# Kernel optimization log

Hardware: AMD Instinct MI355X
Metric: run time of the kernel (lower is better)

Reference implementation:

```python
import jax, jax.numpy as jnp
import numpy as np


def setup_inputs() -> dict:
    key = jax.random.key(0)
    k1, k2 = jax.random.split(key)
    B, d, h = 65536, 256, 1024  # na = d//4 = 64, G = B//na = 1024, h = 4*d
    x = jax.random.normal(k1, (B, d), dtype=jnp.float32)
    A = 0.1 * jax.random.normal(k2, (d, h), dtype=jnp.float32)
    return {"x": x, "A": A}


def reference(x, A):
    # x: [B, d], A: [d, h] with h = 4*d, na = d // 4, G = B // na
    B, d = x.shape
    na = d // 4
    G = B // na
    n2 = 2 * na

    # bmm with broadcast A + SiLU -> [B, h]; reshape [B, 16, na], sum -> [B]
    J = jax.nn.silu(x @ A)                      # [B, h]
    j12 = J.reshape(B, 16, na).sum(axis=(1, 2)).reshape(G, na)  # [G, na]

    # kron(diag(j12), eye(2)) duplicates each diagonal entry onto a 2x2 identity
    diagvals = jnp.repeat(j12, 2, axis=1)        # [G, 2*na]

    # Final block matrix [[J11, J12], [J21, J22]] with J11=J22=0,
    # J12 = +diag, J21 = -diag, each expanded by kron with eye(2).
    idx = jnp.arange(n2)
    out = jnp.zeros((G, 4 * na, 4 * na), dtype=x.dtype)
    out = out.at[:, idx, n2 + idx].set(diagvals)    # top-right block diagonal
    out = out.at[:, n2 + idx, idx].set(-diagvals)   # bottom-left block diagonal
    return out
```

## Files before the change

kernel.cpp:

```cpp
#include <hip/hip_runtime.h>
#include <stdint.h>

typedef float    f32x4  __attribute__((ext_vector_type(4)));
typedef __bf16   bf16x8 __attribute__((ext_vector_type(8)));
typedef uint32_t u32x4  __attribute__((ext_vector_type(4)));
typedef unsigned short u16x4 __attribute__((ext_vector_type(4)));

#define AS1 __attribute__((address_space(1)))
#define AS3 __attribute__((address_space(3)))

__device__ __forceinline__ unsigned short f2bf_bits(float f) {
  uint32_t u = __builtin_bit_cast(uint32_t, f);
  u += 0x7fffu + ((u >> 16) & 1u);
  return (unsigned short)(u >> 16);
}

__global__ void k_transpose_cvt(const float* __restrict__ A,
                                unsigned short* __restrict__ At) {
  int n = blockIdx.x * blockDim.x + threadIdx.x;
  int o = n << 2;
  int col = o >> 8;
  int k   = o & 255;
  u16x4 v;
#pragma unroll
  for (int j = 0; j < 4; ++j) v[j] = f2bf_bits(A[(size_t)(k + j) * 1024 + col]);
  *reinterpret_cast<u16x4*>(At + o) = v;
}

__launch_bounds__(256, 2)
__global__ void k_gemm_fused(const float* __restrict__ x,
                             const unsigned short* __restrict__ At,
                             float* __restrict__ out) {
  __shared__ alignas(16) char lds[8192];

  const int tid  = threadIdx.x;
  const int lane = tid & 63;
  const int w    = tid >> 6;
  const int bIdx = blockIdx.x;
  const int brow = bIdx * 128;

  const int col = lane & 15;
  const int hi  = lane >> 4;

  bf16x8 xf[2][8];
#pragma unroll
  for (int rg = 0; rg < 2; ++rg) {
    const float* xr = x + (size_t)(brow + w * 32 + rg * 16 + col) * 256;
#pragma unroll
    for (int s = 0; s < 8; ++s) {
      f32x4 a = __builtin_nontemporal_load(
          reinterpret_cast<const f32x4*>(xr + s * 32 + hi * 8));
      f32x4 b = __builtin_nontemporal_load(
          reinterpret_cast<const f32x4*>(xr + s * 32 + hi * 8 + 4));
      bf16x8 f;
      f[0] = (__bf16)a[0]; f[1] = (__bf16)a[1];
      f[2] = (__bf16)a[2]; f[3] = (__bf16)a[3];
      f[4] = (__bf16)b[0]; f[5] = (__bf16)b[1];
      f[6] = (__bf16)b[2]; f[7] = (__bf16)b[3];
      xf[rg][s] = f;
    }
  }

  uint32_t p0 = (uint32_t)(w * 2048 + lane * 16);
  uint32_t so0 = p0 ^ (((p0 >> 9) & 7u) << 4);
  uint32_t p1 = p0 + 1024u;
  uint32_t so1 = p1 ^ (((p1 >> 9) & 7u) << 4);
  char* ldsw0 = lds + w * 2048;
  char* ldsw1 = lds + w * 2048 + 1024;

  uint32_t rbase = ((uint32_t)(col * 512 + hi * 16)) ^ ((uint32_t)(col & 7) << 4);

  float sums[2][4] = {{0.f, 0.f, 0.f, 0.f}, {0.f, 0.f, 0.f, 0.f}};
  float* outblk = out + (size_t)bIdx * 131072;
  const f32x4 z4 = {0.f, 0.f, 0.f, 0.f};

  for (int tile = 0; tile < 64; ++tile) {
    const char* tsrc = (const char*)At + (size_t)tile * 8192;
    __builtin_amdgcn_global_load_lds((const AS1 uint32_t*)(tsrc + so0),
                                     (AS3 uint32_t*)ldsw0, 16, 0, 0);
    __builtin_amdgcn_global_load_lds((const AS1 uint32_t*)(tsrc + so1),
                                     (AS3 uint32_t*)ldsw1, 16, 0, 0);

    float* zp = outblk + tile * 2048 + (tid << 2);
    __builtin_nontemporal_store(z4, reinterpret_cast<f32x4*>(zp));
    __builtin_nontemporal_store(z4, reinterpret_cast<f32x4*>(zp + 1024));

    __syncthreads();

    bf16x8 bfr[8];
#pragma unroll
    for (int s = 0; s < 8; ++s) {
      uint32_t addr = rbase ^ ((uint32_t)s << 6);
      bfr[s] = __builtin_bit_cast(
          bf16x8, *reinterpret_cast<const u32x4*>(lds + addr));
    }
    f32x4 acc[2] = {{0.f, 0.f, 0.f, 0.f}, {0.f, 0.f, 0.f, 0.f}};
#pragma unroll
    for (int s = 0; s < 8; ++s) {
      acc[0] = __builtin_amdgcn_mfma_f32_16x16x32_bf16(xf[0][s], bfr[s], acc[0], 0, 0, 0);
      acc[1] = __builtin_amdgcn_mfma_f32_16x16x32_bf16(xf[1][s], bfr[s], acc[1], 0, 0, 0);
    }
#pragma unroll
    for (int rg = 0; rg < 2; ++rg)
#pragma unroll
      for (int j = 0; j < 4; ++j) {
        float z = acc[rg][j];
        float sig = __builtin_amdgcn_rcpf(1.0f + __expf(-z));
        sums[rg][j] += z * sig;
      }
    __syncthreads();
  }

#pragma unroll
  for (int rg = 0; rg < 2; ++rg)
#pragma unroll
    for (int j = 0; j < 4; ++j) {
      float v = sums[rg][j];
      v += __shfl_xor(v, 1, 64);
      v += __shfl_xor(v, 2, 64);
      v += __shfl_xor(v, 4, 64);
      v += __shfl_xor(v, 8, 64);
      sums[rg][j] = v;
    }

  if (col == 0) {
#pragma unroll
    for (int rg = 0; rg < 2; ++rg)
#pragma unroll
      for (int j = 0; j < 4; ++j) {
        int rb_ = brow + w * 32 + rg * 16 + hi * 4 + j;
        int g = rb_ >> 6;
        int c = rb_ & 63;
        float s = sums[rg][j];
        float* og = out + (size_t)g * 65536;
        og[(2 * c) * 256 + 128 + 2 * c]     =  s;
        og[(2 * c + 1) * 256 + 129 + 2 * c] =  s;
        og[(128 + 2 * c) * 256 + 2 * c]     = -s;
        og[(129 + 2 * c) * 256 + 2 * c + 1] = -s;
      }
  }
}

extern "C" void kernel_launch(void* const* d_in, const int* in_sizes, int n_in,
                              void* d_out, int out_size, void* d_ws, size_t ws_size,
                              hipStream_t stream) {
  const float* x = (const float*)d_in[0];
  const float* A = (const float*)d_in[1];
  float* out = (float*)d_out;
  unsigned short* At = (unsigned short*)d_ws;

  k_transpose_cvt<<<256, 256, 0, stream>>>(A, At);
  k_gemm_fused<<<512, 256, 0, stream>>>(x, At, out);
}
```

Before: 79.24 us.

## Multi-buffer A tiles in LDS with two-tile-ahead prefetch

```diff
diff --git a/kernel.cpp b/kernel.cpp
--- a/kernel.cpp
+++ b/kernel.cpp
@@ -31,7 +31,7 @@
 __global__ void k_gemm_fused(const float* __restrict__ x,
                              const unsigned short* __restrict__ At,
                              float* __restrict__ out) {
-  __shared__ alignas(16) char lds[8192];
+  __shared__ alignas(16) char lds[4][8192];
 
   const int tid  = threadIdx.x;
   const int lane = tid & 63;
@@ -41,6 +41,25 @@
 
   const int col = lane & 15;
   const int hi  = lane >> 4;
+
+  uint32_t p0  = (uint32_t)(w * 2048 + lane * 16);
+  uint32_t so0 = p0 ^ (((p0 >> 9) & 7u) << 4);
+  uint32_t p1  = p0 + 1024u;
+  uint32_t so1 = p1 ^ (((p1 >> 9) & 7u) << 4);
+
+  {
+    const char* t0 = (const char*)At;
+    const char* t1 = (const char*)At + 8192;
+    __builtin_amdgcn_global_load_lds((const AS1 uint32_t*)(t0 + so0),
+                                     (AS3 uint32_t*)(lds[0] + w * 2048), 16, 0, 0);
+    __builtin_amdgcn_global_load_lds((const AS1 uint32_t*)(t0 + so1),
+                                     (AS3 uint32_t*)(lds[0] + w * 2048 + 1024), 16, 0, 0);
+    __builtin_amdgcn_global_load_lds((const AS1 uint32_t*)(t1 + so0),
+                                     (AS3 uint32_t*)(lds[1] + w * 2048), 16, 0, 0);
+    __builtin_amdgcn_global_load_lds((const AS1 uint32_t*)(t1 + so1),
+                                     (AS3 uint32_t*)(lds[1] + w * 2048 + 1024), 16, 0, 0);
+  }
+  __builtin_amdgcn_sched_barrier(0);
 
   bf16x8 xf[2][8];
 #pragma unroll
@@ -60,13 +79,7 @@
       xf[rg][s] = f;
     }
   }
-
-  uint32_t p0 = (uint32_t)(w * 2048 + lane * 16);
-  uint32_t so0 = p0 ^ (((p0 >> 9) & 7u) << 4);
-  uint32_t p1 = p0 + 1024u;
-  uint32_t so1 = p1 ^ (((p1 >> 9) & 7u) << 4);
-  char* ldsw0 = lds + w * 2048;
-  char* ldsw1 = lds + w * 2048 + 1024;
+  asm volatile("s_waitcnt vmcnt(0)" ::: "memory");
 
   uint32_t rbase = ((uint32_t)(col * 512 + hi * 16)) ^ ((uint32_t)(col & 7) << 4);
 
@@ -75,24 +88,28 @@
   const f32x4 z4 = {0.f, 0.f, 0.f, 0.f};
 
   for (int tile = 0; tile < 64; ++tile) {
-    const char* tsrc = (const char*)At + (size_t)tile * 8192;
-    __builtin_amdgcn_global_load_lds((const AS1 uint32_t*)(tsrc + so0),
-                                     (AS3 uint32_t*)ldsw0, 16, 0, 0);
-    __builtin_amdgcn_global_load_lds((const AS1 uint32_t*)(tsrc + so1),
-                                     (AS3 uint32_t*)ldsw1, 16, 0, 0);
-
+    {
+      int pt = (tile + 2) & 63;
+      const char* tsrc = (const char*)At + (size_t)pt * 8192;
+      char* dst = lds[(tile + 2) & 3] + w * 2048;
+      __builtin_amdgcn_global_load_lds((const AS1 uint32_t*)(tsrc + so0),
+                                       (AS3 uint32_t*)dst, 16, 0, 0);
+      __builtin_amdgcn_global_load_lds((const AS1 uint32_t*)(tsrc + so1),
+                                       (AS3 uint32_t*)(dst + 1024), 16, 0, 0);
+    }
     float* zp = outblk + tile * 2048 + (tid << 2);
     __builtin_nontemporal_store(z4, reinterpret_cast<f32x4*>(zp));
     __builtin_nontemporal_store(z4, reinterpret_cast<f32x4*>(zp + 1024));
 
-    __syncthreads();
+    asm volatile("s_waitcnt vmcnt(8)\n\ts_barrier" ::: "memory");
 
+    const char* buf = lds[tile & 3];
     bf16x8 bfr[8];
 #pragma unroll
     for (int s = 0; s < 8; ++s) {
       uint32_t addr = rbase ^ ((uint32_t)s << 6);
       bfr[s] = __builtin_bit_cast(
-          bf16x8, *reinterpret_cast<const u32x4*>(lds + addr));
+          bf16x8, *reinterpret_cast<const u32x4*>(buf + addr));
     }
     f32x4 acc[2] = {{0.f, 0.f, 0.f, 0.f}, {0.f, 0.f, 0.f, 0.f}};
 #pragma unroll
@@ -108,8 +125,9 @@
         float sig = __builtin_amdgcn_rcpf(1.0f + __expf(-z));
         sums[rg][j] += z * sig;
       }
-    __syncthreads();
   }
+
+  asm volatile("s_waitcnt vmcnt(0)\n\ts_barrier" ::: "memory");
 
 #pragma unroll
   for (int rg = 0; rg < 2; ++rg)
```

Result: slower. 81.91 us (+3.4%).

## Give each wave its own group and a private 4-deep LDS prefetch ring

Applied to the files above, without the earlier changes.

```diff
diff --git a/kernel.cpp b/kernel.cpp
--- a/kernel.cpp
+++ b/kernel.cpp
@@ -27,112 +27,133 @@
   *reinterpret_cast<u16x4*>(At + o) = v;
 }
 
-__launch_bounds__(256, 2)
-__global__ void k_gemm_fused(const float* __restrict__ x,
-                             const unsigned short* __restrict__ At,
-                             float* __restrict__ out) {
-  __shared__ alignas(16) char lds[8192];
+__launch_bounds__(256, 1)
+__global__ void k_fused(const float* __restrict__ x,
+                        const unsigned short* __restrict__ At,
+                        float* __restrict__ out) {
+  __shared__ alignas(16) char lds[4][4][8192];
 
   const int tid  = threadIdx.x;
   const int lane = tid & 63;
   const int w    = tid >> 6;
-  const int bIdx = blockIdx.x;
-  const int brow = bIdx * 128;
+  const int g    = blockIdx.x * 4 + w;
 
   const int col = lane & 15;
   const int hi  = lane >> 4;
 
-  bf16x8 xf[2][8];
+  uint32_t soff[8];
 #pragma unroll
-  for (int rg = 0; rg < 2; ++rg) {
-    const float* xr = x + (size_t)(brow + w * 32 + rg * 16 + col) * 256;
+  for (int i = 0; i < 8; ++i) {
+    uint32_t p = (uint32_t)(i * 1024 + lane * 16);
+    soff[i] = p ^ (((p >> 9) & 7u) << 4);
+  }
+
+#pragma unroll
+  for (int t = 0; t < 3; ++t) {
+    const char* src = (const char*)At + (size_t)t * 8192;
+    char* dst = lds[w][t];
+#pragma unroll
+    for (int i = 0; i < 8; ++i)
+      __builtin_amdgcn_global_load_lds((const AS1 uint32_t*)(src + soff[i]),
+                                       (AS3 uint32_t*)(dst + i * 1024), 16, 0, 0);
+  }
+  __builtin_amdgcn_sched_barrier(0);
+
+  bf16x8 xf[4][8];
+#pragma unroll
+  for (int r = 0; r < 4; ++r) {
+    const float* xr = x + (size_t)(g * 64 + r * 16 + col) * 256;
 #pragma unroll
     for (int s = 0; s < 8; ++s) {
       f32x4 a = __builtin_nontemporal_load(
           reinterpret_cast<const f32x4*>(xr + s * 32 + hi * 8));
-      f32x4 b = __builtin_nontemporal_load(
+      f32x4 bq = __builtin_nontemporal_load(
           reinterpret_cast<const f32x4*>(xr + s * 32 + hi * 8 + 4));
       bf16x8 f;
-      f[0] = (__bf16)a[0]; f[1] = (__bf16)a[1];
-      f[2] = (__bf16)a[2]; f[3] = (__bf16)a[3];
-      f[4] = (__bf16)b[0]; f[5] = (__bf16)b[1];
-      f[6] = (__bf16)b[2]; f[7] = (__bf16)b[3];
-      xf[rg][s] = f;
+      f[0] = (__bf16)a[0];  f[1] = (__bf16)a[1];
+      f[2] = (__bf16)a[2];  f[3] = (__bf16)a[3];
+      f[4] = (__bf16)bq[0]; f[5] = (__bf16)bq[1];
+      f[6] = (__bf16)bq[2]; f[7] = (__bf16)bq[3];
+      xf[r][s] = f;
     }
   }
-
-  uint32_t p0 = (uint32_t)(w * 2048 + lane * 16);
-  uint32_t so0 = p0 ^ (((p0 >> 9) & 7u) << 4);
-  uint32_t p1 = p0 + 1024u;
-  uint32_t so1 = p1 ^ (((p1 >> 9) & 7u) << 4);
-  char* ldsw0 = lds + w * 2048;
-  char* ldsw1 = lds + w * 2048 + 1024;
+  asm volatile("s_waitcnt vmcnt(0)" ::: "memory");
 
   uint32_t rbase = ((uint32_t)(col * 512 + hi * 16)) ^ ((uint32_t)(col & 7) << 4);
 
-  float sums[2][4] = {{0.f, 0.f, 0.f, 0.f}, {0.f, 0.f, 0.f, 0.f}};
-  float* outblk = out + (size_t)bIdx * 131072;
+  float sums[4][4] = {{0.f,0.f,0.f,0.f},{0.f,0.f,0.f,0.f},
+                      {0.f,0.f,0.f,0.f},{0.f,0.f,0.f,0.f}};
+  float* og = out + (size_t)g * 65536;
   const f32x4 z4 = {0.f, 0.f, 0.f, 0.f};
 
-  for (int tile = 0; tile < 64; ++tile) {
-    const char* tsrc = (const char*)At + (size_t)tile * 8192;
-    __builtin_amdgcn_global_load_lds((const AS1 uint32_t*)(tsrc + so0),
-                                     (AS3 uint32_t*)ldsw0, 16, 0, 0);
-    __builtin_amdgcn_global_load_lds((const AS1 uint32_t*)(tsrc + so1),
-                                     (AS3 uint32_t*)ldsw1, 16, 0, 0);
+  for (int t = 0; t < 64; ++t) {
+    asm volatile("s_waitcnt lgkmcnt(0)" ::: "memory");
+    {
+      int pt = (t + 3) & 63;
+      const char* src = (const char*)At + (size_t)pt * 8192;
+      char* dst = lds[w][(t + 3) & 3];
+#pragma unroll
+      for (int i = 0; i < 8; ++i)
+        __builtin_amdgcn_global_load_lds((const AS1 uint32_t*)(src + soff[i]),
+                                         (AS3 uint32_t*)(dst + i * 1024), 16, 0, 0);
+    }
+    __builtin_amdgcn_sched_barrier(0);
+    {
+      float* zp = og + t * 1024 + lane * 4;
+#pragma unroll
+      for (int q = 0; q < 4; ++q)
+        __builtin_nontemporal_store(z4, reinterpret_cast<f32x4*>(zp + q * 256));
+    }
+    asm volatile("s_waitcnt vmcnt(40)" ::: "memory");
 
-    float* zp = outblk + tile * 2048 + (tid << 2);
-    __builtin_nontemporal_store(z4, reinterpret_cast<f32x4*>(zp));
-    __builtin_nontemporal_store(z4, reinterpret_cast<f32x4*>(zp + 1024));
-
-    __syncthreads();
-
+    const char* buf = lds[w][t & 3];
     bf16x8 bfr[8];
 #pragma unroll
     for (int s = 0; s < 8; ++s) {
       uint32_t addr = rbase ^ ((uint32_t)s << 6);
       bfr[s] = __builtin_bit_cast(
-          bf16x8, *reinterpret_cast<const u32x4*>(lds + addr));
+          bf16x8, *reinterpret_cast<const u32x4*>(buf + addr));
     }
-    f32x4 acc[2] = {{0.f, 0.f, 0.f, 0.f}, {0.f, 0.f, 0.f, 0.f}};
+    f32x4 acc[4] = {{0.f,0.f,0.f,0.f},{0.f,0.f,0.f,0.f},
+                    {0.f,0.f,0.f,0.f},{0.f,0.f,0.f,0.f}};
 #pragma unroll
     for (int s = 0; s < 8; ++s) {
-      acc[0] = __builtin_amdgcn_mfma_f32_16x16x32_bf16(xf[0][s], bfr[s], acc[0], 0, 0, 0);
-      acc[1] = __builtin_amdgcn_mfma_f32_16x16x32_bf16(xf[1][s], bfr[s], acc[1], 0, 0, 0);
+#pragma unroll
+      for (int r = 0; r < 4; ++r)
+        acc[r] = __builtin_amdgcn_mfma_f32_16x16x32_bf16(xf[r][s], bfr[s],
+                                                         acc[r], 0, 0, 0);
     }
 #pragma unroll
-    for (int rg = 0; rg < 2; ++rg)
+    for (int r = 0; r < 4; ++r)
 #pragma unroll
       for (int j = 0; j < 4; ++j) {
-        float z = acc[rg][j];
+        float z = acc[r][j];
         float sig = __builtin_amdgcn_rcpf(1.0f + __expf(-z));
-        sums[rg][j] += z * sig;
+        sums[r][j] += z * sig;
       }
-    __syncthreads();
   }
 
+  asm volatile("s_waitcnt vmcnt(0)" ::: "memory");
+
 #pragma unroll
-  for (int rg = 0; rg < 2; ++rg)
+  for (int r = 0; r < 4; ++r)
 #pragma unroll
     for (int j = 0; j < 4; ++j) {
-      float v = sums[rg][j];
+      float v = sums[r][j];
       v += __shfl_xor(v, 1, 64);
       v += __shfl_xor(v, 2, 64);
       v += __shfl_xor(v, 4, 64);
       v += __shfl_xor(v, 8, 64);
-      sums[rg][j] = v;
+      sums[r][j] = v;
     }
 
   if (col == 0) {
 #pragma unroll
-    for (int rg = 0; rg < 2; ++rg)
+    for (int r = 0; r < 4; ++r)
 #pragma unroll
       for (int j = 0; j < 4; ++j) {
-        int rb_ = brow + w * 32 + rg * 16 + hi * 4 + j;
-        int g = rb_ >> 6;
-        int c = rb_ & 63;
-        float s = sums[rg][j];
-        float* og = out + (size_t)g * 65536;
+        int c = r * 16 + hi * 4 + j;
+        float s = sums[r][j];
         og[(2 * c) * 256 + 128 + 2 * c]     =  s;
         og[(2 * c + 1) * 256 + 129 + 2 * c] =  s;
         og[(128 + 2 * c) * 256 + 2 * c]     = -s;
@@ -150,5 +171,5 @@
   unsigned short* At = (unsigned short*)d_ws;
 
   k_transpose_cvt<<<256, 256, 0, stream>>>(A, At);
-  k_gemm_fused<<<512, 256, 0, stream>>>(x, At, out);
+  k_fused<<<256, 256, 0, stream>>>(x, At, out);
 }
```

Result: no change. 78.19 us (median of 2 runs) (-1.3%).
